# Kernel optimization log

Hardware: AMD Instinct MI355X
Metric: run time of the kernel (lower is better)

## Reference

```python
import jax, jax.numpy as jnp
import numpy as np

LUT_SIZE = 4096
TWO_PI = 2.0 * np.pi


def _lut_tables():
    idx = jnp.arange(LUT_SIZE, dtype=jnp.float32)
    ang = idx * (TWO_PI / LUT_SIZE)
    return jnp.sin(ang), jnp.cos(ang)


def lut_sin_cos(theta):
    """4096-entry LUT sin/cos with linear interpolation, period 2*pi."""
    sin_t, cos_t = _lut_tables()
    fidx = theta * (LUT_SIZE / TWO_PI)
    i0f = jnp.floor(fidx)
    w = fidx - i0f  # interpolation weight in [0,1)
    i0 = jnp.mod(i0f.astype(jnp.int32), LUT_SIZE)
    i1 = jnp.mod(i0 + 1, LUT_SIZE)
    s = sin_t[i0] * (1.0 - w) + sin_t[i1] * w
    c = cos_t[i0] * (1.0 - w) + cos_t[i1] * w
    return s, c


def setup_inputs() -> dict:
    key = jax.random.key(0)
    ks = jax.random.split(key, 9)
    B_, D, N = 32, 1024, 2048
    return {
        "x_real": jax.random.normal(ks[0], (B_, D), jnp.float32),
        "x_imag": jax.random.normal(ks[1], (B_, D), jnp.float32),
        "t": jax.random.uniform(ks[2], (B_,), jnp.float32),
        "input_proj_w": jax.random.normal(ks[3], (D, 2 * D), jnp.float32) * (1.0 / np.sqrt(2 * D)),
        "input_proj_b": jnp.zeros((D,), jnp.float32),
        "W": jax.random.normal(ks[4], (N, D), jnp.float32) * 0.02,
        "B": jnp.zeros((N, D), jnp.float32),
        "out_real_w": jax.random.normal(ks[5], (D, N), jnp.float32) * (1.0 / np.sqrt(N)),
        "out_imag_w": jax.random.normal(ks[6], (D, N), jnp.float32) * (1.0 / np.sqrt(N)),
    }


def reference(x_real, x_imag, t, input_proj_w, input_proj_b, W, B, out_real_w, out_imag_w):
    # input projection on concatenated real/imag: (batch, d_model)
    x_combined = jnp.concatenate([x_real, x_imag], axis=-1)
    x_collapsed = x_combined @ input_proj_w.T + input_proj_b
    # broadcast: (batch, 1, d) / (n, d) + (n, d) + (batch, 1, 1)
    wavelength = 1.0 + jnp.abs(W)
    theta = x_collapsed[:, None, :] / wavelength + B + t[:, None, None]
    sin_theta, cos_theta = lut_sin_cos(theta)
    cos_sum = cos_theta.sum(axis=-1)  # (batch, n)
    sin_sum = sin_theta.sum(axis=-1)
    out_real = cos_sum @ out_real_w.T
    out_imag = sin_sum @ out_imag_w.T
    return jax.nn.silu(out_real), jax.nn.silu(out_imag)
```

## Files before the change

### kernel.cpp

```cpp
#include <hip/hip_runtime.h>
#include <math.h>

#define D_MODEL 1024
#define N_RES   2048
#define BATCH   32
constexpr float INV_2PI = 0.15915494309189535f;

#define WS_XC 0
#define WS_CS (32 * 1024)
#define WS_SS (WS_CS + 32 * 2048)
#define WS_PA (WS_SS + 32 * 2048)
#define WS_PR (WS_PA + 2 * 32 * 1024)
#define WS_PI (WS_PR + 4 * 32 * 1024)

__global__ __launch_bounds__(256) void kA_partial(const float* __restrict__ xr,
                                                  const float* __restrict__ xi,
                                                  const float* __restrict__ ipw,
                                                  float* __restrict__ pa) {
  const int tid  = threadIdx.x;
  const int lane = tid & 63;
  const int wave = tid >> 6;
  const int d0 = (blockIdx.x & 255) * 4;
  const int kc = blockIdx.x >> 8;
  const int b0 = wave * 8;

  const float4* x4p  = (const float4*)(kc ? xi : xr);
  const float4* ipw4 = (const float4*)ipw;
  const int woff = kc * 256;

  float acc[8][4];
#pragma unroll
  for (int b = 0; b < 8; ++b)
#pragma unroll
    for (int d = 0; d < 4; ++d) acc[b][d] = 0.f;

#pragma unroll 1
  for (int i = 0; i < 4; ++i) {
    const int j = lane + 64 * i;
    float4 w4[4];
#pragma unroll
    for (int d = 0; d < 4; ++d) w4[d] = ipw4[(d0 + d) * 512 + woff + j];
#pragma unroll
    for (int b = 0; b < 8; ++b) {
      float4 x4 = x4p[(b0 + b) * 256 + j];
#pragma unroll
      for (int d = 0; d < 4; ++d) {
        acc[b][d] += x4.x * w4[d].x + x4.y * w4[d].y + x4.z * w4[d].z + x4.w * w4[d].w;
      }
    }
  }

#pragma unroll
  for (int b = 0; b < 8; ++b) {
#pragma unroll
    for (int d = 0; d < 4; ++d) {
      float v = acc[b][d];
#pragma unroll
      for (int m = 32; m >= 1; m >>= 1) v += __shfl_xor(v, m, 64);
      if (lane == 0) pa[(size_t)(kc * BATCH + b0 + b) * D_MODEL + d0 + d] = v;
    }
  }
}

__global__ __launch_bounds__(256) void kA2(const float* __restrict__ pa,
                                           const float* __restrict__ bias,
                                           float* __restrict__ xc) {
  const int idx = blockIdx.x * 256 + threadIdx.x;
  const float4* pa4 = (const float4*)pa;
  const float4* b4p = (const float4*)bias;
  float4 a = pa4[idx];
  float4 b = pa4[8192 + idx];
  float4 c = b4p[idx & 255];
  float4 r;
  r.x = a.x + b.x + c.x;
  r.y = a.y + b.y + c.y;
  r.z = a.z + b.z + c.z;
  r.w = a.w + b.w + c.w;
  ((float4*)xc)[idx] = r;
}

__global__ __launch_bounds__(256) void kB(const float* __restrict__ xc,
                                          const float* __restrict__ W,
                                          const float* __restrict__ Bm,
                                          const float* __restrict__ t,
                                          float* __restrict__ cos_sum,
                                          float* __restrict__ sin_sum) {
  __shared__ float a_s[D_MODEL];
  __shared__ float c_s[D_MODEL];
  const int n   = blockIdx.x;
  const int tid = threadIdx.x;

  {
    const float4* W4 = (const float4*)(W + (size_t)n * D_MODEL);
    const float4* B4 = (const float4*)(Bm + (size_t)n * D_MODEL);
    float4 w4 = W4[tid];
    float4 b4 = B4[tid];
    float4 a4, c4;
    a4.x = INV_2PI / (1.f + fabsf(w4.x));
    a4.y = INV_2PI / (1.f + fabsf(w4.y));
    a4.z = INV_2PI / (1.f + fabsf(w4.z));
    a4.w = INV_2PI / (1.f + fabsf(w4.w));
    c4.x = b4.x * INV_2PI;
    c4.y = b4.y * INV_2PI;
    c4.z = b4.z * INV_2PI;
    c4.w = b4.w * INV_2PI;
    ((float4*)a_s)[tid] = a4;
    ((float4*)c_s)[tid] = c4;
  }
  __syncthreads();

  const int lane = tid & 63;
  const int wave = tid >> 6;
  const int b0 = wave * 8;
  const float4* as4 = (const float4*)a_s;
  const float4* cs4 = (const float4*)c_s;

#pragma unroll 1
  for (int bb = 0; bb < 8; ++bb) {
    const int b = b0 + bb;
    const float t2 = t[b] * INV_2PI;
    const float4* x4p = (const float4*)(xc + (size_t)b * D_MODEL);
    float ss = 0.f, cc = 0.f;
#pragma unroll
    for (int i = 0; i < 4; ++i) {
      const int j = lane + 64 * i;
      float4 x4 = x4p[j];
      float4 a4 = as4[j];
      float4 c4 = cs4[j];
      {
        float r = x4.x * a4.x + c4.x + t2;
        float fr = r - floorf(r);
        ss += __builtin_amdgcn_sinf(fr);
        cc += __builtin_amdgcn_cosf(fr);
      }
      {
        float r = x4.y * a4.y + c4.y + t2;
        float fr = r - floorf(r);
        ss += __builtin_amdgcn_sinf(fr);
        cc += __builtin_amdgcn_cosf(fr);
      }
      {
        float r = x4.z * a4.z + c4.z + t2;
        float fr = r - floorf(r);
        ss += __builtin_amdgcn_sinf(fr);
        cc += __builtin_amdgcn_cosf(fr);
      }
      {
        float r = x4.w * a4.w + c4.w + t2;
        float fr = r - floorf(r);
        ss += __builtin_amdgcn_sinf(fr);
        cc += __builtin_amdgcn_cosf(fr);
      }
    }
#pragma unroll
    for (int m = 32; m >= 1; m >>= 1) {
      ss += __shfl_xor(ss, m, 64);
      cc += __shfl_xor(cc, m, 64);
    }
    if (lane == 0) {
      cos_sum[(size_t)b * N_RES + n] = cc;
      sin_sum[(size_t)b * N_RES + n] = ss;
    }
  }
}

__global__ __launch_bounds__(256) void kC_partial(const float* __restrict__ cos_sum,
                                                  const float* __restrict__ sin_sum,
                                                  const float* __restrict__ orw,
                                                  const float* __restrict__ oiw,
                                                  float* __restrict__ pr,
                                                  float* __restrict__ pi) {
  const int tid  = threadIdx.x;
  const int lane = tid & 63;
  const int wave = tid >> 6;
  const int d0 = (blockIdx.x & 255) * 4;
  const int kc = blockIdx.x >> 8;
  const int b0 = wave * 8;
  const int jbase = kc * 128;

  float ar[8][4], ai[8][4];
#pragma unroll
  for (int b = 0; b < 8; ++b)
#pragma unroll
    for (int d = 0; d < 4; ++d) { ar[b][d] = 0.f; ai[b][d] = 0.f; }

#pragma unroll 1
  for (int i = 0; i < 2; ++i) {
    const int j = jbase + lane + 64 * i;
    float4 wr[4], wi[4];
#pragma unroll
    for (int d = 0; d < 4; ++d) {
      wr[d] = ((const float4*)(orw + (size_t)(d0 + d) * N_RES))[j];
      wi[d] = ((const float4*)(oiw + (size_t)(d0 + d) * N_RES))[j];
    }
#pragma unroll
    for (int b = 0; b < 8; ++b) {
      float4 cs = ((const float4*)(cos_sum + (size_t)(b0 + b) * N_RES))[j];
      float4 sn = ((const float4*)(sin_sum + (size_t)(b0 + b) * N_RES))[j];
#pragma unroll
      for (int d = 0; d < 4; ++d) {
        ar[b][d] += cs.x * wr[d].x + cs.y * wr[d].y + cs.z * wr[d].z + cs.w * wr[d].w;
        ai[b][d] += sn.x * wi[d].x + sn.y * wi[d].y + sn.z * wi[d].z + sn.w * wi[d].w;
      }
    }
  }

#pragma unroll
  for (int b = 0; b < 8; ++b) {
#pragma unroll
    for (int d = 0; d < 4; ++d) {
      float vr = ar[b][d];
      float vi = ai[b][d];
#pragma unroll
      for (int m = 32; m >= 1; m >>= 1) {
        vr += __shfl_xor(vr, m, 64);
        vi += __shfl_xor(vi, m, 64);
      }
      if (lane == 0) {
        const size_t o = (size_t)(kc * BATCH + b0 + b) * D_MODEL + d0 + d;
        pr[o] = vr;
        pi[o] = vi;
      }
    }
  }
}

__device__ __forceinline__ float silu(float v) { return v / (1.f + __expf(-v)); }

__global__ __launch_bounds__(256) void kC2(const float* __restrict__ pr,
                                           const float* __restrict__ pi,
                                           float* __restrict__ out) {
  const int idx = blockIdx.x * 256 + threadIdx.x;
  const float4* pr4 = (const float4*)pr;
  const float4* pi4 = (const float4*)pi;
  float4 vr = pr4[idx];
  float4 vi = pi4[idx];
#pragma unroll
  for (int kc = 1; kc < 4; ++kc) {
    float4 a = pr4[kc * 8192 + idx];
    float4 b = pi4[kc * 8192 + idx];
    vr.x += a.x; vr.y += a.y; vr.z += a.z; vr.w += a.w;
    vi.x += b.x; vi.y += b.y; vi.z += b.z; vi.w += b.w;
  }
  float4 orr, oii;
  orr.x = silu(vr.x); orr.y = silu(vr.y); orr.z = silu(vr.z); orr.w = silu(vr.w);
  oii.x = silu(vi.x); oii.y = silu(vi.y); oii.z = silu(vi.z); oii.w = silu(vi.w);
  ((float4*)out)[idx] = orr;
  ((float4*)out)[8192 + idx] = oii;
}

extern "C" void kernel_launch(void* const* d_in, const int* in_sizes, int n_in,
                              void* d_out, int out_size, void* d_ws, size_t ws_size,
                              hipStream_t stream) {
  const float* xr   = (const float*)d_in[0];
  const float* xi   = (const float*)d_in[1];
  const float* t    = (const float*)d_in[2];
  const float* ipw  = (const float*)d_in[3];
  const float* bias = (const float*)d_in[4];
  const float* W    = (const float*)d_in[5];
  const float* Bm   = (const float*)d_in[6];
  const float* orw  = (const float*)d_in[7];
  const float* oiw  = (const float*)d_in[8];
  float* out = (float*)d_out;

  float* ws      = (float*)d_ws;
  float* xc      = ws + WS_XC;
  float* cos_sum = ws + WS_CS;
  float* sin_sum = ws + WS_SS;
  float* pa      = ws + WS_PA;
  float* pr      = ws + WS_PR;
  float* pi      = ws + WS_PI;

  kA_partial<<<512, 256, 0, stream>>>(xr, xi, ipw, pa);
  kA2<<<32, 256, 0, stream>>>(pa, bias, xc);
  kB<<<N_RES, 256, 0, stream>>>(xc, W, Bm, t, cos_sum, sin_sum);
  kC_partial<<<1024, 256, 0, stream>>>(cos_sum, sin_sum, orw, oiw, pr, pi);
  kC2<<<32, 256, 0, stream>>>(pr, pi, out);
}
```

Measured before the change: 165.1 us.

## Fuse split-K reductions into GEMV kernels and use butterfly shuffle reductions

Drops the split-K partial kernels and their combine passes, so the input projection adds the bias directly and the output projection applies SiLU directly, going from five launches to three. Cross-lane reductions become butterfly transposes that reduce many accumulators together, replacing one full shuffle tree per value. The phase kernel handles two resonators per block, so each xc load is reused twice, and it uses v_fract and fma. Fewer, larger blocks (256 blocks of 512 threads) may reduce parallelism for the GEMV stages.

```diff
diff --git a/kernel.cpp b/kernel.cpp
--- a/kernel.cpp
+++ b/kernel.cpp
@@ -7,76 +7,93 @@
 constexpr float INV_2PI = 0.15915494309189535f;
 
 #define WS_XC 0
-#define WS_CS (32 * 1024)
-#define WS_SS (WS_CS + 32 * 2048)
-#define WS_PA (WS_SS + 32 * 2048)
-#define WS_PR (WS_PA + 2 * 32 * 1024)
-#define WS_PI (WS_PR + 4 * 32 * 1024)
-
-__global__ __launch_bounds__(256) void kA_partial(const float* __restrict__ xr,
-                                                  const float* __restrict__ xi,
-                                                  const float* __restrict__ ipw,
-                                                  float* __restrict__ pa) {
+#define WS_CS (BATCH * D_MODEL)
+#define WS_SS (WS_CS + BATCH * N_RES)
+
+template <int V>
+__device__ __forceinline__ void bstage(float* acc, int lane, int m) {
+  const bool hi = (lane & m) != 0;
+#pragma unroll
+  for (int v = 0; v < V / 2; ++v) {
+    float send = hi ? acc[v] : acc[v + V / 2];
+    float keep = hi ? acc[v + V / 2] : acc[v];
+    acc[v] = keep + __shfl_xor(send, m, 64);
+  }
+}
+
+__device__ __forceinline__ float silu(float v) { return v / (1.f + __expf(-v)); }
+
+__global__ __launch_bounds__(512) void kA(const float* __restrict__ xr,
+                                          const float* __restrict__ xi,
+                                          const float* __restrict__ ipw,
+                                          const float* __restrict__ bias,
+                                          float* __restrict__ xc) {
   const int tid  = threadIdx.x;
   const int lane = tid & 63;
   const int wave = tid >> 6;
-  const int d0 = (blockIdx.x & 255) * 4;
-  const int kc = blockIdx.x >> 8;
-  const int b0 = wave * 8;
-
-  const float4* x4p  = (const float4*)(kc ? xi : xr);
+  const int d0 = blockIdx.x * 4;
+  const int b0 = wave * 4;
+
+  const float4* xr4  = (const float4*)xr;
+  const float4* xi4  = (const float4*)xi;
   const float4* ipw4 = (const float4*)ipw;
-  const int woff = kc * 256;
-
-  float acc[8][4];
-#pragma unroll
-  for (int b = 0; b < 8; ++b)
-#pragma unroll
-    for (int d = 0; d < 4; ++d) acc[b][d] = 0.f;
-
-#pragma unroll 1
+
+  float acc[16];
+#pragma unroll
+  for (int v = 0; v < 16; ++v) acc[v] = 0.f;
+
+#pragma unroll 2
   for (int i = 0; i < 4; ++i) {
     const int j = lane + 64 * i;
-    float4 w4[4];
-#pragma unroll
-    for (int d = 0; d < 4; ++d) w4[d] = ipw4[(d0 + d) * 512 + woff + j];
-#pragma unroll
-    for (int b = 0; b < 8; ++b) {
-      float4 x4 = x4p[(b0 + b) * 256 + j];
-#pragma unroll
-      for (int d = 0; d < 4; ++d) {
-        acc[b][d] += x4.x * w4[d].x + x4.y * w4[d].y + x4.z * w4[d].z + x4.w * w4[d].w;
-      }
-    }
-  }
-
-#pragma unroll
-  for (int b = 0; b < 8; ++b) {
-#pragma unroll
-    for (int d = 0; d < 4; ++d) {
-      float v = acc[b][d];
-#pragma unroll
-      for (int m = 32; m >= 1; m >>= 1) v += __shfl_xor(v, m, 64);
-      if (lane == 0) pa[(size_t)(kc * BATCH + b0 + b) * D_MODEL + d0 + d] = v;
-    }
-  }
-}
-
-__global__ __launch_bounds__(256) void kA2(const float* __restrict__ pa,
-                                           const float* __restrict__ bias,
-                                           float* __restrict__ xc) {
-  const int idx = blockIdx.x * 256 + threadIdx.x;
-  const float4* pa4 = (const float4*)pa;
-  const float4* b4p = (const float4*)bias;
-  float4 a = pa4[idx];
-  float4 b = pa4[8192 + idx];
-  float4 c = b4p[idx & 255];
-  float4 r;
-  r.x = a.x + b.x + c.x;
-  r.y = a.y + b.y + c.y;
-  r.z = a.z + b.z + c.z;
-  r.w = a.w + b.w + c.w;
-  ((float4*)xc)[idx] = r;
+    float4 w4[4], x4[4];
+#pragma unroll
+    for (int d = 0; d < 4; ++d) w4[d] = ipw4[(d0 + d) * 512 + j];
+#pragma unroll
+    for (int b = 0; b < 4; ++b) x4[b] = xr4[(b0 + b) * 256 + j];
+#pragma unroll
+    for (int b = 0; b < 4; ++b)
+#pragma unroll
+      for (int d = 0; d < 4; ++d)
+        acc[(b << 2) | d] += x4[b].x * w4[d].x + x4[b].y * w4[d].y +
+                             x4[b].z * w4[d].z + x4[b].w * w4[d].w;
+  }
+#pragma unroll 2
+  for (int i = 0; i < 4; ++i) {
+    const int j = lane + 64 * i;
+    float4 w4[4], x4[4];
+#pragma unroll
+    for (int d = 0; d < 4; ++d) w4[d] = ipw4[(d0 + d) * 512 + 256 + j];
+#pragma unroll
+    for (int b = 0; b < 4; ++b) x4[b] = xi4[(b0 + b) * 256 + j];
+#pragma unroll
+    for (int b = 0; b < 4; ++b)
+#pragma unroll
+      for (int d = 0; d < 4; ++d)
+        acc[(b << 2) | d] += x4[b].x * w4[d].x + x4[b].y * w4[d].y +
+                             x4[b].z * w4[d].z + x4[b].w * w4[d].w;
+  }
+
+  bstage<16>(acc, lane, 32);
+  bstage<8>(acc, lane, 16);
+  bstage<4>(acc, lane, 8);
+  bstage<2>(acc, lane, 4);
+  float r = acc[0];
+  r += __shfl_xor(r, 2, 64);
+  r += __shfl_xor(r, 1, 64);
+  if ((lane & 3) == 0) {
+    const int b = (lane >> 4) & 3;
+    const int d = (lane >> 2) & 3;
+    xc[(size_t)(b0 + b) * D_MODEL + d0 + d] = r + bias[d0 + d];
+  }
+}
+
+__device__ __forceinline__ void sc1(float xv, float av, float cv, float t2,
+                                    float& ca, float& sa) {
+  float r = __builtin_fmaf(xv, av, cv + t2);
+  float fr;
+  asm("v_fract_f32 %0, %1" : "=v"(fr) : "v"(r));
+  sa += __builtin_amdgcn_sinf(fr);
+  ca += __builtin_amdgcn_cosf(fr);
 }
 
 __global__ __launch_bounds__(256) void kB(const float* __restrict__ xc,
@@ -85,16 +102,15 @@
                                           const float* __restrict__ t,
                                           float* __restrict__ cos_sum,
                                           float* __restrict__ sin_sum) {
-  __shared__ float a_s[D_MODEL];
-  __shared__ float c_s[D_MODEL];
-  const int n   = blockIdx.x;
+  __shared__ float a_s[2][D_MODEL];
+  __shared__ float c_s[2][D_MODEL];
+  const int n0  = blockIdx.x * 2;
   const int tid = threadIdx.x;
 
-  {
-    const float4* W4 = (const float4*)(W + (size_t)n * D_MODEL);
-    const float4* B4 = (const float4*)(Bm + (size_t)n * D_MODEL);
-    float4 w4 = W4[tid];
-    float4 b4 = B4[tid];
+#pragma unroll
+  for (int rr = 0; rr < 2; ++rr) {
+    float4 w4 = ((const float4*)(W + (size_t)(n0 + rr) * D_MODEL))[tid];
+    float4 b4 = ((const float4*)(Bm + (size_t)(n0 + rr) * D_MODEL))[tid];
     float4 a4, c4;
     a4.x = INV_2PI / (1.f + fabsf(w4.x));
     a4.y = INV_2PI / (1.f + fabsf(w4.y));
@@ -104,8 +120,8 @@
     c4.y = b4.y * INV_2PI;
     c4.z = b4.z * INV_2PI;
     c4.w = b4.w * INV_2PI;
-    ((float4*)a_s)[tid] = a4;
-    ((float4*)c_s)[tid] = c4;
+    ((float4*)a_s[rr])[tid] = a4;
+    ((float4*)c_s[rr])[tid] = c4;
   }
   __syncthreads();
 
@@ -120,133 +136,93 @@
     const int b = b0 + bb;
     const float t2 = t[b] * INV_2PI;
     const float4* x4p = (const float4*)(xc + (size_t)b * D_MODEL);
-    float ss = 0.f, cc = 0.f;
+    float acc[4] = {0.f, 0.f, 0.f, 0.f};
 #pragma unroll
     for (int i = 0; i < 4; ++i) {
       const int j = lane + 64 * i;
       float4 x4 = x4p[j];
-      float4 a4 = as4[j];
-      float4 c4 = cs4[j];
-      {
-        float r = x4.x * a4.x + c4.x + t2;
-        float fr = r - floorf(r);
-        ss += __builtin_amdgcn_sinf(fr);
-        cc += __builtin_amdgcn_cosf(fr);
+#pragma unroll
+      for (int rr = 0; rr < 2; ++rr) {
+        float4 a4 = as4[rr * 256 + j];
+        float4 c4 = cs4[rr * 256 + j];
+        sc1(x4.x, a4.x, c4.x, t2, acc[rr], acc[2 + rr]);
+        sc1(x4.y, a4.y, c4.y, t2, acc[rr], acc[2 + rr]);
+        sc1(x4.z, a4.z, c4.z, t2, acc[rr], acc[2 + rr]);
+        sc1(x4.w, a4.w, c4.w, t2, acc[rr], acc[2 + rr]);
       }
-      {
-        float r = x4.y * a4.y + c4.y + t2;
-        float fr = r - floorf(r);
-        ss += __builtin_amdgcn_sinf(fr);
-        cc += __builtin_amdgcn_cosf(fr);
-      }
-      {
-        float r = x4.z * a4.z + c4.z + t2;
-        float fr = r - floorf(r);
-        ss += __builtin_amdgcn_sinf(fr);
-        cc += __builtin_amdgcn_cosf(fr);
-      }
-      {
-        float r = x4.w * a4.w + c4.w + t2;
-        float fr = r - floorf(r);
-        ss += __builtin_amdgcn_sinf(fr);
-        cc += __builtin_amdgcn_cosf(fr);
-      }
-    }
-#pragma unroll
-    for (int m = 32; m >= 1; m >>= 1) {
-      ss += __shfl_xor(ss, m, 64);
-      cc += __shfl_xor(cc, m, 64);
-    }
-    if (lane == 0) {
-      cos_sum[(size_t)b * N_RES + n] = cc;
-      sin_sum[(size_t)b * N_RES + n] = ss;
-    }
-  }
-}
-
-__global__ __launch_bounds__(256) void kC_partial(const float* __restrict__ cos_sum,
-                                                  const float* __restrict__ sin_sum,
-                                                  const float* __restrict__ orw,
-                                                  const float* __restrict__ oiw,
-                                                  float* __restrict__ pr,
-                                                  float* __restrict__ pi) {
+    }
+    bstage<4>(acc, lane, 32);
+    bstage<2>(acc, lane, 16);
+    float v0 = acc[0];
+    v0 += __shfl_xor(v0, 8, 64);
+    v0 += __shfl_xor(v0, 4, 64);
+    v0 += __shfl_xor(v0, 2, 64);
+    v0 += __shfl_xor(v0, 1, 64);
+    if ((lane & 15) == 0) {
+      const int sc = (lane >> 5) & 1;
+      const int rr = (lane >> 4) & 1;
+      float* dst = sc ? sin_sum : cos_sum;
+      dst[(size_t)b * N_RES + n0 + rr] = v0;
+    }
+  }
+}
+
+__global__ __launch_bounds__(512) void kC(const float* __restrict__ cos_sum,
+                                          const float* __restrict__ sin_sum,
+                                          const float* __restrict__ orw,
+                                          const float* __restrict__ oiw,
+                                          float* __restrict__ out) {
   const int tid  = threadIdx.x;
   const int lane = tid & 63;
   const int wave = tid >> 6;
-  const int d0 = (blockIdx.x & 255) * 4;
-  const int kc = blockIdx.x >> 8;
-  const int b0 = wave * 8;
-  const int jbase = kc * 128;
-
-  float ar[8][4], ai[8][4];
-#pragma unroll
-  for (int b = 0; b < 8; ++b)
-#pragma unroll
-    for (int d = 0; d < 4; ++d) { ar[b][d] = 0.f; ai[b][d] = 0.f; }
-
-#pragma unroll 1
-  for (int i = 0; i < 2; ++i) {
-    const int j = jbase + lane + 64 * i;
-    float4 wr[4], wi[4];
+  const int d0 = blockIdx.x * 4;
+  const int b0 = wave * 4;
+
+  const float4* cs4p = (const float4*)cos_sum;
+  const float4* sn4p = (const float4*)sin_sum;
+  const float4* orw4 = (const float4*)orw;
+  const float4* oiw4 = (const float4*)oiw;
+
+  float acc[32];
+#pragma unroll
+  for (int v = 0; v < 32; ++v) acc[v] = 0.f;
+
+#pragma unroll 2
+  for (int i = 0; i < 8; ++i) {
+    const int j = lane + 64 * i;
+    float4 cs[4], sn[4];
+#pragma unroll
+    for (int b = 0; b < 4; ++b) {
+      cs[b] = cs4p[(b0 + b) * 512 + j];
+      sn[b] = sn4p[(b0 + b) * 512 + j];
+    }
 #pragma unroll
     for (int d = 0; d < 4; ++d) {
-      wr[d] = ((const float4*)(orw + (size_t)(d0 + d) * N_RES))[j];
-      wi[d] = ((const float4*)(oiw + (size_t)(d0 + d) * N_RES))[j];
-    }
-#pragma unroll
-    for (int b = 0; b < 8; ++b) {
-      float4 cs = ((const float4*)(cos_sum + (size_t)(b0 + b) * N_RES))[j];
-      float4 sn = ((const float4*)(sin_sum + (size_t)(b0 + b) * N_RES))[j];
-#pragma unroll
-      for (int d = 0; d < 4; ++d) {
-        ar[b][d] += cs.x * wr[d].x + cs.y * wr[d].y + cs.z * wr[d].z + cs.w * wr[d].w;
-        ai[b][d] += sn.x * wi[d].x + sn.y * wi[d].y + sn.z * wi[d].z + sn.w * wi[d].w;
+      float4 wr = orw4[(d0 + d) * 512 + j];
+      float4 wi = oiw4[(d0 + d) * 512 + j];
+#pragma unroll
+      for (int b = 0; b < 4; ++b) {
+        acc[(b << 2) | d] += cs[b].x * wr.x + cs[b].y * wr.y +
+                             cs[b].z * wr.z + cs[b].w * wr.w;
+        acc[16 | (b << 2) | d] += sn[b].x * wi.x + sn[b].y * wi.y +
+                                  sn[b].z * wi.z + sn[b].w * wi.w;
       }
     }
   }
 
-#pragma unroll
-  for (int b = 0; b < 8; ++b) {
-#pragma unroll
-    for (int d = 0; d < 4; ++d) {
-      float vr = ar[b][d];
-      float vi = ai[b][d];
-#pragma unroll
-      for (int m = 32; m >= 1; m >>= 1) {
-        vr += __shfl_xor(vr, m, 64);
-        vi += __shfl_xor(vi, m, 64);
-      }
-      if (lane == 0) {
-        const size_t o = (size_t)(kc * BATCH + b0 + b) * D_MODEL + d0 + d;
-        pr[o] = vr;
-        pi[o] = vi;
-      }
-    }
-  }
-}
-
-__device__ __forceinline__ float silu(float v) { return v / (1.f + __expf(-v)); }
-
-__global__ __launch_bounds__(256) void kC2(const float* __restrict__ pr,
-                                           const float* __restrict__ pi,
-                                           float* __restrict__ out) {
-  const int idx = blockIdx.x * 256 + threadIdx.x;
-  const float4* pr4 = (const float4*)pr;
-  const float4* pi4 = (const float4*)pi;
-  float4 vr = pr4[idx];
-  float4 vi = pi4[idx];
-#pragma unroll
-  for (int kc = 1; kc < 4; ++kc) {
-    float4 a = pr4[kc * 8192 + idx];
-    float4 b = pi4[kc * 8192 + idx];
-    vr.x += a.x; vr.y += a.y; vr.z += a.z; vr.w += a.w;
-    vi.x += b.x; vi.y += b.y; vi.z += b.z; vi.w += b.w;
-  }
-  float4 orr, oii;
-  orr.x = silu(vr.x); orr.y = silu(vr.y); orr.z = silu(vr.z); orr.w = silu(vr.w);
-  oii.x = silu(vi.x); oii.y = silu(vi.y); oii.z = silu(vi.z); oii.w = silu(vi.w);
-  ((float4*)out)[idx] = orr;
-  ((float4*)out)[8192 + idx] = oii;
+  bstage<32>(acc, lane, 32);
+  bstage<16>(acc, lane, 16);
+  bstage<8>(acc, lane, 8);
+  bstage<4>(acc, lane, 4);
+  bstage<2>(acc, lane, 2);
+  float v = acc[0] + __shfl_xor(acc[0], 1, 64);
+  if ((lane & 1) == 0) {
+    const int comp = (lane >> 5) & 1;
+    const int b = (lane >> 3) & 3;
+    const int d = (lane >> 1) & 3;
+    const size_t o = (size_t)(b0 + b) * D_MODEL + d0 + d;
+    out[(size_t)comp * (BATCH * D_MODEL) + o] = silu(v);
+  }
 }
 
 extern "C" void kernel_launch(void* const* d_in, const int* in_sizes, int n_in,
@@ -267,13 +243,8 @@
   float* xc      = ws + WS_XC;
   float* cos_sum = ws + WS_CS;
   float* sin_sum = ws + WS_SS;
-  float* pa      = ws + WS_PA;
-  float* pr      = ws + WS_PR;
-  float* pi      = ws + WS_PI;
-
-  kA_partial<<<512, 256, 0, stream>>>(xr, xi, ipw, pa);
-  kA2<<<32, 256, 0, stream>>>(pa, bias, xc);
-  kB<<<N_RES, 256, 0, stream>>>(xc, W, Bm, t, cos_sum, sin_sum);
-  kC_partial<<<1024, 256, 0, stream>>>(cos_sum, sin_sum, orw, oiw, pr, pi);
-  kC2<<<32, 256, 0, stream>>>(pr, pi, out);
-}
+
+  kA<<<256, 512, 0, stream>>>(xr, xi, ipw, bias, xc);
+  kB<<<N_RES / 2, 256, 0, stream>>>(xc, W, Bm, t, cos_sum, sin_sum);
+  kC<<<256, 512, 0, stream>>>(cos_sum, sin_sum, orw, oiw, out);
+}
```

After: 138.5 us. 16.1% less time.
